# Performance work log

Hardware: AMD Instinct MI355X
Metric: run time of the kernel (lower is better)

The kernel has to match this reference:

```python
import jax, jax.numpy as jnp
import numpy as np

H = W = 64      # patch grid (shape)
WS = 8          # window_size
SHIFT = 4       # shift_size (SW-MSA)
HEAD_DIM = 32
N = WS * WS     # tokens per window


def _rel_position_index(ws):
    coords = np.stack(np.meshgrid(np.arange(ws), np.arange(ws), indexing='ij'))  # (2, ws, ws)
    cf = coords.reshape(2, -1)
    rel = cf[:, :, None] - cf[:, None, :]            # (2, N, N)
    rel = rel.transpose(1, 2, 0).astype(np.int64)    # (N, N, 2)
    rel[..., 0] += ws - 1
    rel[..., 1] += ws - 1
    rel[..., 0] *= 2 * ws - 1
    return (rel[..., 0] + rel[..., 1]).astype(np.int32)  # (N, N), values in [0,(2ws-1)^2)


def _shift_mask(h, w, ws, shift):
    # Swin cyclic-shift attention mask: (num_windows, N, N) with 0 / -100
    img = np.zeros((h, w), dtype=np.float32)
    cnt = 0
    slices = (slice(0, -ws), slice(-ws, -shift), slice(-shift, None))
    for hs in slices:
        for ws_ in slices:
            img[hs, ws_] = cnt
            cnt += 1
    win = img.reshape(h // ws, ws, w // ws, ws).transpose(0, 2, 1, 3).reshape(-1, ws * ws)
    diff = win[:, None, :] - win[:, :, None]
    return np.where(diff != 0, np.float32(-100.0), np.float32(0.0))


def setup_inputs() -> dict:
    key = jax.random.key(0)
    ks = jax.random.split(key, 6)
    dim = 384
    B = 32
    sd = 1.0 / np.sqrt(dim)
    return {
        'x': jax.random.normal(ks[0], (B, H * W, dim), jnp.float32),
        'qkv_w': jax.random.normal(ks[1], (dim, 3 * dim), jnp.float32) * sd,
        'qkv_b': jnp.zeros((3 * dim,), jnp.float32),
        'proj_w': jax.random.normal(ks[2], (dim, dim), jnp.float32) * sd,
        'proj_b': jnp.zeros((dim,), jnp.float32),
        'bias_table': jax.random.normal(ks[3], ((2 * WS - 1) ** 2, dim // HEAD_DIM), jnp.float32) * 0.02,
        'rel_index': jnp.asarray(_rel_position_index(WS)),
    }


def reference(x, qkv_w, qkv_b, proj_w, proj_b, bias_table, rel_index):
    B, L, C = x.shape
    heads = C // HEAD_DIM
    scale = HEAD_DIM ** -0.5
    nh, nw = H // WS, W // WS

    xg = x.reshape(B, H, W, C)
    if SHIFT > 0:
        xg = jnp.roll(xg, shift=(-SHIFT, -SHIFT), axis=(1, 2))

    # window partition -> (B*nWin, N, C)
    xw = xg.reshape(B, nh, WS, nw, WS, C).transpose(0, 1, 3, 2, 4, 5).reshape(B * nh * nw, N, C)

    qkv = xw @ qkv_w + qkv_b                              # (Bw, N, 3C)
    q, k, v = jnp.split(qkv, 3, axis=-1)
    def heads_first(t):
        return t.reshape(-1, N, heads, HEAD_DIM).transpose(0, 2, 1, 3)  # (Bw, h, N, d)
    q, k, v = heads_first(q), heads_first(k), heads_first(v)

    attn = jnp.einsum('bhnd,bhmd->bhnm', q * scale, k)    # (Bw, h, N, N)
    bias = bias_table[rel_index]                          # (N, N, h)
    attn = attn + bias.transpose(2, 0, 1)[None]

    if SHIFT > 0:
        mask = jnp.asarray(_shift_mask(H, W, WS, SHIFT))  # (nWin, N, N), trace-time constant
        attn = attn.reshape(B, nh * nw, heads, N, N) + mask[None, :, None]
        attn = attn.reshape(B * nh * nw, heads, N, N)

    attn = jax.nn.softmax(attn, axis=-1)
    out = jnp.einsum('bhnm,bhmd->bhnd', attn, v)          # (Bw, h, N, d)
    out = out.transpose(0, 2, 1, 3).reshape(B * nh * nw, N, C)
    out = out @ proj_w + proj_b

    # window reverse
    out = out.reshape(B, nh, nw, WS, WS, C).transpose(0, 1, 3, 2, 4, 5).reshape(B, H, W, C)
    if SHIFT > 0:
        out = jnp.roll(out, shift=(SHIFT, SHIFT), axis=(1, 2))
    return out.reshape(B, L, C)
```

## Files before the change

### kernel.cpp

```cpp
#include <hip/hip_runtime.h>
#include <hip/hip_bf16.h>

#define CDIM 384
#define NQKV 1152
#define HEADS 12
#define SHIFT_ 4
#define SCALE_Q 0.17677669529663687f

typedef __attribute__((ext_vector_type(8))) short bf16x8;
typedef __attribute__((ext_vector_type(4))) float f32x4;
typedef __attribute__((ext_vector_type(4))) float float4_t;
typedef __attribute__((ext_vector_type(4))) unsigned u32x4;
typedef __attribute__((ext_vector_type(2))) unsigned u32x2;

__device__ inline short f2bf(float f) {
    union { float f; unsigned u; } v; v.f = f;
    unsigned r = v.u + 0x7FFFu + ((v.u >> 16) & 1u);
    return (short)(r >> 16);
}

__device__ inline unsigned cvtpk(float lo, float hi) {
    unsigned r;
    asm("v_cvt_pk_bf16_f32 %0, %1, %2" : "=v"(r) : "v"(lo), "v"(hi));
    return r;
}

__device__ inline bf16x8 mk8(unsigned w0, unsigned w1, unsigned w2, unsigned w3) {
    u32x4 t = {w0, w1, w2, w3};
    return __builtin_bit_cast(bf16x8, t);
}

__device__ inline bf16x8 regroup(unsigned p0, unsigned p1, unsigned p2,
                                 unsigned p3, int lane) {
    int lhi = (lane >> 4) & 3;
    int s0 = (lane & 15) + ((lhi & 1) ? 32 : 0);
    int s1 = s0 + 16;
    unsigned a0 = __shfl(p0, s0), b0 = __shfl(p2, s0);
    unsigned a1 = __shfl(p1, s0), b1 = __shfl(p3, s0);
    unsigned a2 = __shfl(p0, s1), b2 = __shfl(p2, s1);
    unsigned a3 = __shfl(p1, s1), b3 = __shfl(p3, s1);
    bool hi = lhi >= 2;
    return mk8(hi ? b0 : a0, hi ? b1 : a1, hi ? b2 : a2, hi ? b3 : a3);
}

__device__ inline void gl16(const short* g, const short* l) {
    __builtin_amdgcn_global_load_lds((const __attribute__((address_space(1))) void*)g,
                                     (__attribute__((address_space(3))) void*)l, 16, 0, 0);
}

__device__ inline int invswz(int c) {
    int b2 = (c >> 2) & 1, b3 = (c >> 3) & 1, b4 = (c >> 4) & 1;
    return (c & ~7) | ((b2 ^ b4) << 2) | (((((c >> 1) & 1)) ^ b3) << 1) | ((c & 1) ^ b2 ^ b4);
}

__device__ inline int region_id(int wIdx, int tok) {
    int gh = ((wIdx >> 3) << 3) + (tok >> 3);
    int gw = (wIdx & 7) * 8 + (tok & 7);
    int rh = gh < 56 ? 0 : (gh < 60 ? 1 : 2);
    int rw = gw < 56 ? 0 : (gw < 60 ? 1 : 2);
    return rh * 3 + rw;
}

__global__ void prep_kernel(const float* __restrict__ qkv_w,
                            const float* __restrict__ proj_w,
                            const float* __restrict__ bias_table,
                            const int* __restrict__ rel_index,
                            short* __restrict__ qkvwt,
                            short* __restrict__ projwt,
                            float* __restrict__ biasP) {
    int t = blockIdx.x * 256 + threadIdx.x;
    if (t < NQKV * CDIM) {
        int n = t / CDIM, k = t - n * CDIM;
        qkvwt[t] = f2bf(qkv_w[k * NQKV + n]);
    }
    if (t < CDIM * CDIM) {
        int n = t / CDIM, k = t - n * CDIM;
        projwt[t] = f2bf(proj_w[k * CDIM + n]);
    }
    if (t < HEADS * 16 * 64 * 4) {
        int r = t & 3, lane = (t >> 2) & 63, g = (t >> 8) & 15, h = t >> 12;
        int kt = g >> 2, qt = g & 3;
        int key = kt * 16 + (lane >> 4) * 4 + r;
        int query = qt * 16 + (lane & 15);
        biasP[t] = bias_table[rel_index[query * 64 + key] * HEADS + h];
    }
}

__global__ __launch_bounds__(256) void xwin_kernel(const float* __restrict__ x,
                                                   short* __restrict__ xw) {
    int t = blockIdx.x * 256 + threadIdx.x;
    int mg = t / 48;
    int col = (t - mg * 48) * 8;
    int tok = mg & 63, win = mg >> 6;
    int b = win >> 6, wIdx = win & 63;
    int gh = ((wIdx >> 3) << 3) + (tok >> 3);
    int gw = (wIdx & 7) * 8 + (tok & 7);
    int sh_ = (gh + SHIFT_) & 63, sw_ = (gw + SHIFT_) & 63;
    const float* src = x + (size_t)(b * 4096 + sh_ * 64 + sw_) * CDIM + col;
    float4_t a0 = __builtin_nontemporal_load((const float4_t*)src);
    float4_t a1 = __builtin_nontemporal_load((const float4_t*)(src + 4));
    bf16x8 o;
    #pragma unroll
    for (int i = 0; i < 4; i++) { o[i] = f2bf(a0[i]); o[4 + i] = f2bf(a1[i]); }
    __builtin_nontemporal_store(o, (bf16x8*)(xw + (size_t)t * 8));
}

__global__ __launch_bounds__(256) void gemm_qkv(
    const short* __restrict__ xw, const short* __restrict__ wt,
    const float* __restrict__ qkv_b, short* __restrict__ qkbuf,
    short* __restrict__ vT)
{
    __shared__ alignas(16) short smem[128 * 136];
    short* As = smem;
    short* Bs = smem + 4096;
    int tid = threadIdx.x;
    int hw = blockIdx.x;
    int lb = (hw & 7) * 1152 + (hw >> 3);
    int bm = lb / 9, bn = lb - bm * 9;
    int m0 = bm * 128, n0 = bn * 128;

    int lane = tid & 63, wv = tid >> 6;
    int c0 = wv * 128 + lane, c1 = c0 + 64;
    int l0 = invswz(c0), l1 = invswz(c1);
    const short* Ag0 = xw + (size_t)(m0 + (l0 >> 2)) * CDIM + (l0 & 3) * 8;
    const short* Ag1 = xw + (size_t)(m0 + (l1 >> 2)) * CDIM + (l1 & 3) * 8;
    const short* Bg0 = wt + (size_t)(n0 + (l0 >> 2)) * CDIM + (l0 & 3) * 8;
    const short* Bg1 = wt + (size_t)(n0 + (l1 >> 2)) * CDIM + (l1 & 3) * 8;
    const short* Adst0 = (const short*)((const char*)As + wv * 2048);
    const short* Adst1 = (const short*)((const char*)As + wv * 2048 + 1024);
    const short* Bdst0 = (const short*)((const char*)Bs + wv * 2048);
    const short* Bdst1 = (const short*)((const char*)Bs + wv * 2048 + 1024);

    int wr = wv >> 1, wc = wv & 1;
    int lrow = lane & 15, lhi = lane >> 4;
    int arow = wr * 64 + lrow, brow = wc * 64 + lrow;
    const short* ard = As + ((((arow * 64 + lhi * 16)) ^ ((lrow & 7) << 4)) >> 1);
    const short* brd = Bs + ((((brow * 64 + lhi * 16)) ^ ((lrow & 7) << 4)) >> 1);

    f32x4 zero = {0.f, 0.f, 0.f, 0.f};
    f32x4 acc[4][4];
    #pragma unroll
    for (int i = 0; i < 4; i++)
        #pragma unroll
        for (int j = 0; j < 4; j++) acc[i][j] = zero;

    for (int k0 = 0; k0 < CDIM; k0 += 32) {
        gl16(Ag0 + k0, Adst0);
        gl16(Bg0 + k0, Bdst0);
        gl16(Ag1 + k0, Adst1);
        gl16(Bg1 + k0, Bdst1);
        __syncthreads();
        bf16x8 af[4], bfr[4];
        #pragma unroll
        for (int t = 0; t < 4; t++) af[t]  = *(const bf16x8*)(ard + t * 512);
        #pragma unroll
        for (int t = 0; t < 4; t++) bfr[t] = *(const bf16x8*)(brd + t * 512);
        #pragma unroll
        for (int i = 0; i < 4; i++)
            #pragma unroll
            for (int j = 0; j < 4; j++)
                acc[i][j] = __builtin_amdgcn_mfma_f32_16x16x32_bf16(af[i], bfr[j], acc[i][j], 0, 0, 0);
        __syncthreads();
    }
    #pragma unroll
    for (int tj = 0; tj < 4; tj++) {
        int col = wc * 64 + tj * 16 + lrow;
        int cg = n0 + col;
        float bias = qkv_b[cg];
        float sc = (cg < CDIM) ? SCALE_Q : 1.0f;
        #pragma unroll
        for (int ti = 0; ti < 4; ti++) {
            int row0 = wr * 64 + ti * 16 + lhi * 4;
            #pragma unroll
            for (int r = 0; r < 4; r++)
                smem[(row0 + r) * 136 + col] = f2bf((acc[ti][tj][r] + bias) * sc);
        }
    }
    __syncthreads();
    if (bn < 6) {
        #pragma unroll
        for (int i = 0; i < 8; i++) {
            int rr = i * 16 + (tid >> 4);
            int cc = (tid & 15) * 8;
            bf16x8 v = *(const bf16x8*)(smem + rr * 136 + cc);
            __builtin_nontemporal_store(v,
                (bf16x8*)(qkbuf + (size_t)(m0 + rr) * 768 + n0 + cc));
        }
    } else {
        #pragma unroll
        for (int it = 0; it < 8; it++) {
            int t = it * 256 + tid;
            int col = t >> 4, tk8 = t & 15;
            bf16x8 v;
            #pragma unroll
            for (int j = 0; j < 8; j++)
                v[j] = smem[(tk8 * 8 + j) * 136 + col];
            int win = bm * 2 + (tk8 >> 3);
            int head = (bn - 6) * 4 + (col >> 5);
            int dim = col & 31;
            __builtin_nontemporal_store(v,
                (bf16x8*)(vT + (((size_t)win * HEADS + head) * 32 + dim) * 64 + (tk8 & 7) * 8));
        }
    }
}

__global__ __launch_bounds__(256) void attn_reg(
    const short* __restrict__ qkbuf, const short* __restrict__ vT,
    const float* __restrict__ biasP, short* __restrict__ attno)
{
    int tid = threadIdx.x;
    int lane = tid & 63, wv = tid >> 6;
    int lrow = lane & 15, lhi = lane >> 4;
    int w = blockIdx.x;
    int wIdx = w & 63;
    bool needmask = ((wIdx >> 3) == 7) || ((wIdx & 7) == 7);

    int rq[4], rk[4][4];
    #pragma unroll
    for (int qt = 0; qt < 4; qt++) rq[qt] = region_id(wIdx, qt * 16 + lrow);
    #pragma unroll
    for (int kt = 0; kt < 4; kt++)
        #pragma unroll
        for (int r = 0; r < 4; r++)
            rk[kt][r] = region_id(wIdx, kt * 16 + lhi * 4 + r);

    f32x4 zero = {0.f, 0.f, 0.f, 0.f};
    const short* qbase = qkbuf + (size_t)(w * 64) * 768;

    for (int hi = 0; hi < 3; hi++) {
        int h = wv * 3 + hi;
        bf16x8 kf[4];
        #pragma unroll
        for (int kt = 0; kt < 4; kt++)
            kf[kt] = __builtin_nontemporal_load(
                (const bf16x8*)(qbase + (size_t)(kt * 16 + lrow) * 768 + CDIM + h * 32 + lhi * 8));
        bf16x8 pa[4][2];
        #pragma unroll
        for (int qt = 0; qt < 4; qt++) {
            bf16x8 qf = __builtin_nontemporal_load(
                (const bf16x8*)(qbase + (size_t)(qt * 16 + lrow) * 768 + h * 32 + lhi * 8));
            f32x4 st[4];
            __builtin_amdgcn_s_setprio(1);
            #pragma unroll
            for (int kt = 0; kt < 4; kt++)
                st[kt] = __builtin_amdgcn_mfma_f32_16x16x32_bf16(kf[kt], qf, zero, 0, 0, 0);
            __builtin_amdgcn_s_setprio(0);
            float pv[16]; float sum = 0.f;
            #pragma unroll
            for (int kt = 0; kt < 4; kt++) {
                f32x4 bb = *(const f32x4*)(biasP + (((size_t)h * 16 + kt * 4 + qt) * 64 + lane) * 4);
                #pragma unroll
                for (int r = 0; r < 4; r++) {
                    float p = __expf(st[kt][r] + bb[r]);
                    p = (needmask && (rq[qt] != rk[kt][r])) ? 0.f : p;
                    pv[kt * 4 + r] = p; sum += p;
                }
            }
            sum += __shfl_xor(sum, 16);
            sum += __shfl_xor(sum, 32);
            float rcp = 1.0f / sum;
            unsigned a0 = cvtpk(pv[0] * rcp, pv[1] * rcp);
            unsigned a1 = cvtpk(pv[2] * rcp, pv[3] * rcp);
            unsigned a2 = cvtpk(pv[4] * rcp, pv[5] * rcp);
            unsigned a3 = cvtpk(pv[6] * rcp, pv[7] * rcp);
            pa[qt][0] = regroup(a0, a1, a2, a3, lane);
            a0 = cvtpk(pv[8] * rcp,  pv[9] * rcp);
            a1 = cvtpk(pv[10] * rcp, pv[11] * rcp);
            a2 = cvtpk(pv[12] * rcp, pv[13] * rcp);
            a3 = cvtpk(pv[14] * rcp, pv[15] * rcp);
            pa[qt][1] = regroup(a0, a1, a2, a3, lane);
        }
        const short* vb = vT + ((size_t)w * HEADS + h) * 32 * 64;
        bf16x8 vfrag[2][2];
        #pragma unroll
        for (int ks2 = 0; ks2 < 2; ks2++)
            #pragma unroll
            for (int dt = 0; dt < 2; dt++)
                vfrag[ks2][dt] = __builtin_nontemporal_load(
                    (const bf16x8*)(vb + (size_t)(dt * 16 + lrow) * 64 + ks2 * 32 + lhi * 8));
        f32x4 ao2[4][2];
        #pragma unroll
        for (int qt = 0; qt < 4; qt++) { ao2[qt][0] = zero; ao2[qt][1] = zero; }
        __builtin_amdgcn_s_setprio(1);
        #pragma unroll
        for (int ks2 = 0; ks2 < 2; ks2++)
            #pragma unroll
            for (int qt = 0; qt < 4; qt++) {
                ao2[qt][0] = __builtin_amdgcn_mfma_f32_16x16x32_bf16(vfrag[ks2][0], pa[qt][ks2], ao2[qt][0], 0, 0, 0);
                ao2[qt][1] = __builtin_amdgcn_mfma_f32_16x16x32_bf16(vfrag[ks2][1], pa[qt][ks2], ao2[qt][1], 0, 0, 0);
            }
        __builtin_amdgcn_s_setprio(0);
        short* abase = attno + (size_t)(w * 64) * CDIM + h * 32 + lhi * 4;
        #pragma unroll
        for (int qt = 0; qt < 4; qt++) {
            int token = qt * 16 + lrow;
            short* p0 = abase + (size_t)token * CDIM;
            u32x2 s0, s1;
            s0[0] = cvtpk(ao2[qt][0][0], ao2[qt][0][1]);
            s0[1] = cvtpk(ao2[qt][0][2], ao2[qt][0][3]);
            s1[0] = cvtpk(ao2[qt][1][0], ao2[qt][1][1]);
            s1[1] = cvtpk(ao2[qt][1][2], ao2[qt][1][3]);
            __builtin_nontemporal_store(s0, (u32x2*)(p0));
            __builtin_nontemporal_store(s1, (u32x2*)(p0 + 16));
        }
    }
}

__global__ __launch_bounds__(256) void gemm_proj(
    const short* __restrict__ a, const short* __restrict__ wt,
    const float* __restrict__ proj_b, float* __restrict__ out)
{
    __shared__ alignas(16) short As[4096];
    __shared__ alignas(16) short Bs[4096];
    int tid = threadIdx.x;
    int hw = blockIdx.x;
    int lb = (hw & 7) * 384 + (hw >> 3);
    int bm = lb / 3, bn = lb - bm * 3;
    int m0 = bm * 128, n0 = bn * 128;

    int lane = tid & 63, wv = tid >> 6;
    int c0 = wv * 128 + lane, c1 = c0 + 64;
    int l0 = invswz(c0), l1 = invswz(c1);
    const short* Ag0 = a + (size_t)(m0 + (l0 >> 2)) * CDIM + (l0 & 3) * 8;
    const short* Ag1 = a + (size_t)(m0 + (l1 >> 2)) * CDIM + (l1 & 3) * 8;
    const short* Bg0 = wt + (size_t)(n0 + (l0 >> 2)) * CDIM + (l0 & 3) * 8;
    const short* Bg1 = wt + (size_t)(n0 + (l1 >> 2)) * CDIM + (l1 & 3) * 8;
    const short* Adst0 = (const short*)((const char*)As + wv * 2048);
    const short* Adst1 = (const short*)((const char*)As + wv * 2048 + 1024);
    const short* Bdst0 = (const short*)((const char*)Bs + wv * 2048);
    const short* Bdst1 = (const short*)((const char*)Bs + wv * 2048 + 1024);

    int wr = wv >> 1, wc = wv & 1;
    int lrow = lane & 15, lhi = lane >> 4;
    int arow = wr * 64 + lrow, brow = wc * 64 + lrow;
    const short* ard = As + ((((arow * 64 + lhi * 16)) ^ ((lrow & 7) << 4)) >> 1);
    const short* brd = Bs + ((((brow * 64 + lhi * 16)) ^ ((lrow & 7) << 4)) >> 1);

    f32x4 zero = {0.f, 0.f, 0.f, 0.f};
    f32x4 acc[4][4];
    #pragma unroll
    for (int i = 0; i < 4; i++)
        #pragma unroll
        for (int j = 0; j < 4; j++) acc[i][j] = zero;

    for (int k0 = 0; k0 < CDIM; k0 += 32) {
        gl16(Ag0 + k0, Adst0);
        gl16(Bg0 + k0, Bdst0);
        gl16(Ag1 + k0, Adst1);
        gl16(Bg1 + k0, Bdst1);
        __syncthreads();
        bf16x8 af[4], bfr[4];
        #pragma unroll
        for (int t = 0; t < 4; t++) af[t]  = *(const bf16x8*)(ard + t * 512);
        #pragma unroll
        for (int t = 0; t < 4; t++) bfr[t] = *(const bf16x8*)(brd + t * 512);
        #pragma unroll
        for (int i = 0; i < 4; i++)
            #pragma unroll
            for (int j = 0; j < 4; j++)
                acc[i][j] = __builtin_amdgcn_mfma_f32_16x16x32_bf16(af[i], bfr[j], acc[i][j], 0, 0, 0);
        __syncthreads();
    }
    #pragma unroll
    for (int ti = 0; ti < 4; ti++) {
        #pragma unroll
        for (int r = 0; r < 4; r++) {
            int m = m0 + wr * 64 + ti * 16 + lhi * 4 + r;
            int b = m >> 12, wIdx = (m >> 6) & 63, tok = m & 63;
            int gh = ((wIdx >> 3) << 3) + (tok >> 3);
            int gw = (wIdx & 7) * 8 + (tok & 7);
            int ih = (gh + SHIFT_) & 63, iw = (gw + SHIFT_) & 63;
            size_t ob = ((size_t)(b << 12) + ih * 64 + iw) * CDIM;
            #pragma unroll
            for (int tj = 0; tj < 4; tj++) {
                int col = n0 + wc * 64 + tj * 16 + lrow;
                float v = acc[ti][tj][r] + proj_b[col];
                __builtin_nontemporal_store(v, &out[ob + col]);
            }
        }
    }
}

extern "C" void kernel_launch(void* const* d_in, const int* in_sizes, int n_in,
                              void* d_out, int out_size, void* d_ws, size_t ws_size,
                              hipStream_t stream) {
    const float* x          = (const float*)d_in[0];
    const float* qkv_w      = (const float*)d_in[1];
    const float* qkv_b      = (const float*)d_in[2];
    const float* proj_w     = (const float*)d_in[3];
    const float* proj_b     = (const float*)d_in[4];
    const float* bias_table = (const float*)d_in[5];
    const int*   rel_index  = (const int*)d_in[6];
    float* out = (float*)d_out;
    char* ws = (char*)d_ws;

    short* qkvwt = (short*)(ws);
    short* projwt = (short*)(ws + 884736);
    float* biasP  = (float*)(ws + 1179648);
    short* xw     = (short*)(ws + 1376256);
    short* qkbuf  = (short*)(ws + 102039552);
    short* vT     = (short*)(ws + 303366144);
    short* attno  = (short*)(ws + 404029440);

    prep_kernel<<<1728, 256, 0, stream>>>(qkv_w, proj_w, bias_table, rel_index,
                                          qkvwt, projwt, biasP);
    xwin_kernel<<<24576, 256, 0, stream>>>(x, xw);
    gemm_qkv<<<9216, 256, 0, stream>>>(xw, qkvwt, qkv_b, qkbuf, vT);
    attn_reg<<<2048, 256, 0, stream>>>(qkbuf, vT, biasP, attno);
    gemm_proj<<<3072, 256, 0, stream>>>(attno, projwt, proj_b, out);
}
```

Measured before the change: 497.8 us.

## Deepen QKV GEMM K-tile to 128 and pad the C staging rows

The QKV GEMM now loads four 32-wide K slices per stage into a 64KB LDS buffer. This cuts the barriers per output tile from 24 to 6, and the MFMA blocks are wrapped in s_setprio. The C-staging layout adds 8 shorts of padding every 8 rows to reduce LDS bank conflicts on the transposed V reads. The bigger LDS footprint lowers occupancy per CU, and each stage is still loaded and then consumed with no double buffering.

```diff
diff --git a/kernel.cpp b/kernel.cpp
--- a/kernel.cpp
+++ b/kernel.cpp
@@ -60,6 +60,8 @@
     int rw = gw < 56 ? 0 : (gw < 60 ? 1 : 2);
     return rh * 3 + rw;
 }
+
+__device__ inline int crow(int row) { return row * 136 + (row >> 3) * 8; }
 
 __global__ void prep_kernel(const float* __restrict__ qkv_w,
                             const float* __restrict__ proj_w,
@@ -110,9 +112,10 @@
     const float* __restrict__ qkv_b, short* __restrict__ qkbuf,
     short* __restrict__ vT)
 {
-    __shared__ alignas(16) short smem[128 * 136];
-    short* As = smem;
-    short* Bs = smem + 4096;
+    __shared__ alignas(16) char smemb[65536];
+    short* As = (short*)smemb;
+    short* Bs = As + 16384;
+    short* Cst = (short*)smemb;
     int tid = threadIdx.x;
     int hw = blockIdx.x;
     int lb = (hw & 7) * 1152 + (hw >> 3);
@@ -126,10 +129,10 @@
     const short* Ag1 = xw + (size_t)(m0 + (l1 >> 2)) * CDIM + (l1 & 3) * 8;
     const short* Bg0 = wt + (size_t)(n0 + (l0 >> 2)) * CDIM + (l0 & 3) * 8;
     const short* Bg1 = wt + (size_t)(n0 + (l1 >> 2)) * CDIM + (l1 & 3) * 8;
-    const short* Adst0 = (const short*)((const char*)As + wv * 2048);
-    const short* Adst1 = (const short*)((const char*)As + wv * 2048 + 1024);
-    const short* Bdst0 = (const short*)((const char*)Bs + wv * 2048);
-    const short* Bdst1 = (const short*)((const char*)Bs + wv * 2048 + 1024);
+    short* Adst0 = As + wv * 1024;
+    short* Adst1 = Adst0 + 512;
+    short* Bdst0 = Bs + wv * 1024;
+    short* Bdst1 = Bdst0 + 512;
 
     int wr = wv >> 1, wc = wv & 1;
     int lrow = lane & 15, lhi = lane >> 4;
@@ -144,22 +147,30 @@
         #pragma unroll
         for (int j = 0; j < 4; j++) acc[i][j] = zero;
 
-    for (int k0 = 0; k0 < CDIM; k0 += 32) {
-        gl16(Ag0 + k0, Adst0);
-        gl16(Bg0 + k0, Bdst0);
-        gl16(Ag1 + k0, Adst1);
-        gl16(Bg1 + k0, Bdst1);
+    for (int k0 = 0; k0 < CDIM; k0 += 128) {
+        #pragma unroll
+        for (int j = 0; j < 4; j++) {
+            gl16(Ag0 + k0 + j * 32, Adst0 + j * 4096);
+            gl16(Ag1 + k0 + j * 32, Adst1 + j * 4096);
+            gl16(Bg0 + k0 + j * 32, Bdst0 + j * 4096);
+            gl16(Bg1 + k0 + j * 32, Bdst1 + j * 4096);
+        }
         __syncthreads();
-        bf16x8 af[4], bfr[4];
-        #pragma unroll
-        for (int t = 0; t < 4; t++) af[t]  = *(const bf16x8*)(ard + t * 512);
-        #pragma unroll
-        for (int t = 0; t < 4; t++) bfr[t] = *(const bf16x8*)(brd + t * 512);
-        #pragma unroll
-        for (int i = 0; i < 4; i++)
-            #pragma unroll
-            for (int j = 0; j < 4; j++)
-                acc[i][j] = __builtin_amdgcn_mfma_f32_16x16x32_bf16(af[i], bfr[j], acc[i][j], 0, 0, 0);
+        #pragma unroll
+        for (int kk = 0; kk < 4; kk++) {
+            bf16x8 af[4], bfr[4];
+            #pragma unroll
+            for (int t = 0; t < 4; t++) af[t]  = *(const bf16x8*)(ard + kk * 4096 + t * 512);
+            #pragma unroll
+            for (int t = 0; t < 4; t++) bfr[t] = *(const bf16x8*)(brd + kk * 4096 + t * 512);
+            __builtin_amdgcn_s_setprio(1);
+            #pragma unroll
+            for (int i = 0; i < 4; i++)
+                #pragma unroll
+                for (int j = 0; j < 4; j++)
+                    acc[i][j] = __builtin_amdgcn_mfma_f32_16x16x32_bf16(af[i], bfr[j], acc[i][j], 0, 0, 0);
+            __builtin_amdgcn_s_setprio(0);
+        }
         __syncthreads();
     }
     #pragma unroll
@@ -173,7 +184,7 @@
             int row0 = wr * 64 + ti * 16 + lhi * 4;
             #pragma unroll
             for (int r = 0; r < 4; r++)
-                smem[(row0 + r) * 136 + col] = f2bf((acc[ti][tj][r] + bias) * sc);
+                Cst[crow(row0 + r) + col] = f2bf((acc[ti][tj][r] + bias) * sc);
         }
     }
     __syncthreads();
@@ -182,7 +193,7 @@
         for (int i = 0; i < 8; i++) {
             int rr = i * 16 + (tid >> 4);
             int cc = (tid & 15) * 8;
-            bf16x8 v = *(const bf16x8*)(smem + rr * 136 + cc);
+            bf16x8 v = *(const bf16x8*)(Cst + crow(rr) + cc);
             __builtin_nontemporal_store(v,
                 (bf16x8*)(qkbuf + (size_t)(m0 + rr) * 768 + n0 + cc));
         }
@@ -194,7 +205,7 @@
             bf16x8 v;
             #pragma unroll
             for (int j = 0; j < 8; j++)
-                v[j] = smem[(tk8 * 8 + j) * 136 + col];
+                v[j] = Cst[crow(tk8 * 8 + j) + col];
             int win = bm * 2 + (tk8 >> 3);
             int head = (bn - 6) * 4 + (col >> 5);
             int dim = col & 31;
```

New measurement: 512.4 us. +2.9%, slower.

## Fuse shifted window partition and bf16 cast into QKV GEMM A-tile load

Applied to the files above, without the earlier changes.

Drops the separate xwin kernel. The QKV GEMM now reads fp32 x directly through the cyclic-shift and window index mapping, converts it to bf16 with packed cvt instructions, and writes it into swizzled LDS. This removes the intermediate bf16 xw buffer round trip and one kernel launch. In exchange, A tiles are fetched as fp32 through registers instead of async global-to-LDS loads, which doubles A bytes per tile and serializes the loads before the barrier. The epilogue staging also gains row padding to reduce LDS bank conflicts.

```diff
diff --git a/kernel.cpp b/kernel.cpp
--- a/kernel.cpp
+++ b/kernel.cpp
@@ -28,6 +28,11 @@
 __device__ inline bf16x8 mk8(unsigned w0, unsigned w1, unsigned w2, unsigned w3) {
     u32x4 t = {w0, w1, w2, w3};
     return __builtin_bit_cast(bf16x8, t);
+}
+
+__device__ inline bf16x8 pack8(float4_t a, float4_t b) {
+    return mk8(cvtpk(a[0], a[1]), cvtpk(a[2], a[3]),
+               cvtpk(b[0], b[1]), cvtpk(b[2], b[3]));
 }
 
 __device__ inline bf16x8 regroup(unsigned p0, unsigned p1, unsigned p2,
@@ -61,6 +66,17 @@
     return rh * 3 + rw;
 }
 
+__device__ inline int crow(int row) { return row * 136 + (row >> 3) * 8; }
+
+__device__ inline size_t xrow(int mg) {
+    int tok = mg & 63, win = mg >> 6;
+    int b = win >> 6, wIdx = win & 63;
+    int gh = ((wIdx >> 3) << 3) + (tok >> 3);
+    int gw = (wIdx & 7) * 8 + (tok & 7);
+    int sh_ = (gh + SHIFT_) & 63, sw_ = (gw + SHIFT_) & 63;
+    return (size_t)(b * 4096 + sh_ * 64 + sw_) * CDIM;
+}
+
 __global__ void prep_kernel(const float* __restrict__ qkv_w,
                             const float* __restrict__ proj_w,
                             const float* __restrict__ bias_table,
@@ -86,33 +102,15 @@
     }
 }
 
-__global__ __launch_bounds__(256) void xwin_kernel(const float* __restrict__ x,
-                                                   short* __restrict__ xw) {
-    int t = blockIdx.x * 256 + threadIdx.x;
-    int mg = t / 48;
-    int col = (t - mg * 48) * 8;
-    int tok = mg & 63, win = mg >> 6;
-    int b = win >> 6, wIdx = win & 63;
-    int gh = ((wIdx >> 3) << 3) + (tok >> 3);
-    int gw = (wIdx & 7) * 8 + (tok & 7);
-    int sh_ = (gh + SHIFT_) & 63, sw_ = (gw + SHIFT_) & 63;
-    const float* src = x + (size_t)(b * 4096 + sh_ * 64 + sw_) * CDIM + col;
-    float4_t a0 = __builtin_nontemporal_load((const float4_t*)src);
-    float4_t a1 = __builtin_nontemporal_load((const float4_t*)(src + 4));
-    bf16x8 o;
-    #pragma unroll
-    for (int i = 0; i < 4; i++) { o[i] = f2bf(a0[i]); o[4 + i] = f2bf(a1[i]); }
-    __builtin_nontemporal_store(o, (bf16x8*)(xw + (size_t)t * 8));
-}
-
 __global__ __launch_bounds__(256) void gemm_qkv(
-    const short* __restrict__ xw, const short* __restrict__ wt,
+    const float* __restrict__ x, const short* __restrict__ wt,
     const float* __restrict__ qkv_b, short* __restrict__ qkbuf,
     short* __restrict__ vT)
 {
-    __shared__ alignas(16) short smem[128 * 136];
-    short* As = smem;
-    short* Bs = smem + 4096;
+    __shared__ alignas(16) char smemb[35072];
+    short* As = (short*)smemb;
+    short* Bs = As + 4096;
+    short* Cst = (short*)smemb;
     int tid = threadIdx.x;
     int hw = blockIdx.x;
     int lb = (hw & 7) * 1152 + (hw >> 3);
@@ -121,13 +119,13 @@
 
     int lane = tid & 63, wv = tid >> 6;
     int c0 = wv * 128 + lane, c1 = c0 + 64;
+    const float* Asrc0 = x + xrow(m0 + (c0 >> 2)) + (c0 & 3) * 8;
+    const float* Asrc1 = x + xrow(m0 + (c1 >> 2)) + (c1 & 3) * 8;
+    short* Aw0 = As + (c0 ^ ((c0 >> 2) & 7)) * 8;
+    short* Aw1 = As + (c1 ^ ((c1 >> 2) & 7)) * 8;
     int l0 = invswz(c0), l1 = invswz(c1);
-    const short* Ag0 = xw + (size_t)(m0 + (l0 >> 2)) * CDIM + (l0 & 3) * 8;
-    const short* Ag1 = xw + (size_t)(m0 + (l1 >> 2)) * CDIM + (l1 & 3) * 8;
     const short* Bg0 = wt + (size_t)(n0 + (l0 >> 2)) * CDIM + (l0 & 3) * 8;
     const short* Bg1 = wt + (size_t)(n0 + (l1 >> 2)) * CDIM + (l1 & 3) * 8;
-    const short* Adst0 = (const short*)((const char*)As + wv * 2048);
-    const short* Adst1 = (const short*)((const char*)As + wv * 2048 + 1024);
     const short* Bdst0 = (const short*)((const char*)Bs + wv * 2048);
     const short* Bdst1 = (const short*)((const char*)Bs + wv * 2048 + 1024);
 
@@ -144,11 +142,17 @@
         #pragma unroll
         for (int j = 0; j < 4; j++) acc[i][j] = zero;
 
-    for (int k0 = 0; k0 < CDIM; k0 += 32) {
-        gl16(Ag0 + k0, Adst0);
+    #pragma unroll
+    for (int ks = 0; ks < 12; ks++) {
+        int k0 = ks * 32;
+        float4_t a00 = *(const float4_t*)(Asrc0 + k0);
+        float4_t a01 = *(const float4_t*)(Asrc0 + k0 + 4);
+        float4_t a10 = *(const float4_t*)(Asrc1 + k0);
+        float4_t a11 = *(const float4_t*)(Asrc1 + k0 + 4);
         gl16(Bg0 + k0, Bdst0);
-        gl16(Ag1 + k0, Adst1);
         gl16(Bg1 + k0, Bdst1);
+        *(bf16x8*)Aw0 = pack8(a00, a01);
+        *(bf16x8*)Aw1 = pack8(a10, a11);
         __syncthreads();
         bf16x8 af[4], bfr[4];
         #pragma unroll
@@ -173,7 +177,7 @@
             int row0 = wr * 64 + ti * 16 + lhi * 4;
             #pragma unroll
             for (int r = 0; r < 4; r++)
-                smem[(row0 + r) * 136 + col] = f2bf((acc[ti][tj][r] + bias) * sc);
+                Cst[crow(row0 + r) + col] = f2bf((acc[ti][tj][r] + bias) * sc);
         }
     }
     __syncthreads();
@@ -182,7 +186,7 @@
         for (int i = 0; i < 8; i++) {
             int rr = i * 16 + (tid >> 4);
             int cc = (tid & 15) * 8;
-            bf16x8 v = *(const bf16x8*)(smem + rr * 136 + cc);
+            bf16x8 v = *(const bf16x8*)(Cst + crow(rr) + cc);
             __builtin_nontemporal_store(v,
                 (bf16x8*)(qkbuf + (size_t)(m0 + rr) * 768 + n0 + cc));
         }
@@ -194,7 +198,7 @@
             bf16x8 v;
             #pragma unroll
             for (int j = 0; j < 8; j++)
-                v[j] = smem[(tk8 * 8 + j) * 136 + col];
+                v[j] = Cst[crow(tk8 * 8 + j) + col];
             int win = bm * 2 + (tk8 >> 3);
             int head = (bn - 6) * 4 + (col >> 5);
             int dim = col & 31;
@@ -397,15 +401,13 @@
     short* qkvwt = (short*)(ws);
     short* projwt = (short*)(ws + 884736);
     float* biasP  = (float*)(ws + 1179648);
-    short* xw     = (short*)(ws + 1376256);
-    short* qkbuf  = (short*)(ws + 102039552);
-    short* vT     = (short*)(ws + 303366144);
-    short* attno  = (short*)(ws + 404029440);
+    short* qkbuf  = (short*)(ws + 1376256);
+    short* vT     = (short*)(ws + 202702848);
+    short* attno  = (short*)(ws + 303366144);
 
     prep_kernel<<<1728, 256, 0, stream>>>(qkv_w, proj_w, bias_table, rel_index,
                                           qkvwt, projwt, biasP);
-    xwin_kernel<<<24576, 256, 0, stream>>>(x, xw);
-    gemm_qkv<<<9216, 256, 0, stream>>>(xw, qkvwt, qkv_b, qkbuf, vT);
+    gemm_qkv<<<9216, 256, 0, stream>>>(x, qkvwt, qkv_b, qkbuf, vT);
     attn_reg<<<2048, 256, 0, stream>>>(qkbuf, vT, biasP, attno);
     gemm_proj<<<3072, 256, 0, stream>>>(attno, projwt, proj_b, out);
 }
```

Result: faster. 471.6 us (-5.3%).
